# Kernel optimization log

Hardware: AMD Instinct MI355X
Metric: run time of the kernel (lower is better)

## Reference

```python
import jax, jax.numpy as jnp
import numpy as np

EMB_DIM = 128
WEIGHT_COL = 24

def setup_inputs() -> dict:
    key = jax.random.key(0)
    ks = jax.random.split(key, 9)
    B, S = 8, 4096
    s_in = 1.0 / np.sqrt(EMB_DIM)
    s_out = 1.0 / np.sqrt(WEIGHT_COL)
    return {
        "x": jax.random.normal(ks[0], (B, S, EMB_DIM), dtype=jnp.float32),
        "wQ": jax.random.uniform(ks[1], (EMB_DIM, WEIGHT_COL), jnp.float32, -s_in, s_in),
        "bQ": jax.random.uniform(ks[2], (WEIGHT_COL,), jnp.float32, -s_in, s_in),
        "wK": jax.random.uniform(ks[3], (EMB_DIM, WEIGHT_COL), jnp.float32, -s_in, s_in),
        "bK": jax.random.uniform(ks[4], (WEIGHT_COL,), jnp.float32, -s_in, s_in),
        "wV": jax.random.uniform(ks[5], (EMB_DIM, WEIGHT_COL), jnp.float32, -s_in, s_in),
        "bV": jax.random.uniform(ks[6], (WEIGHT_COL,), jnp.float32, -s_in, s_in),
        "wO": jax.random.uniform(ks[7], (WEIGHT_COL, EMB_DIM), jnp.float32, -s_out, s_out),
        "bO": jax.random.uniform(ks[8], (EMB_DIM,), jnp.float32, -s_out, s_out),
    }

def reference(x, wQ, bQ, wK, bK, wV, bV, wO, bO):
    # projections: [B,S,E] -> [B,S,D]
    Q = x @ wQ + bQ
    K = x @ wK + bK
    V = x @ wV + bV
    # NOTE: source scales by sqrt(emb_dim), not sqrt(weight_col)
    scale = 1.0 / np.sqrt(EMB_DIM).astype(np.float32)
    scores = jnp.einsum('bqd,bkd->bqk', Q, K) * scale  # [B,S,S]
    A = jax.nn.softmax(scores, axis=-1)
    H = jnp.einsum('bqk,bkd->bqd', A, V)               # [B,S,D]
    return H @ wO + bO                                  # [B,S,E]
```

## Files before the change

kernel.cpp:

```cpp
#include <hip/hip_runtime.h>
#include <hip/hip_fp16.h>


#define B_ 8
#define S_ 4096
#define E_ 128
#define D_ 24
#define N_ (B_ * S_)
#define SCALE 0.08838834764831845f
#define LOG2E 1.4426950408889634f

#define TK 128
#define KS_STRIDE 40
#define VS_STRIDE 136
#define HS_STRIDE 40
#define XS_STRIDE 136
#define OS_STRIDE 84

typedef __attribute__((ext_vector_type(8))) short bfrag;
typedef __attribute__((ext_vector_type(4))) float ffrag;

__device__ inline unsigned short f2bf(float f) {
    unsigned int x = __builtin_bit_cast(unsigned int, f);
    return (unsigned short)((x + 0x7fffu + ((x >> 16) & 1u)) >> 16);
}
__device__ inline unsigned int pack2h(float a, float b) {
    unsigned int ua = __builtin_bit_cast(unsigned int, a) + 0x8000u;
    unsigned int ub = __builtin_bit_cast(unsigned int, b) + 0x8000u;
    return __builtin_amdgcn_perm(ub, ua, 0x07060302);
}
__device__ inline unsigned int packh16(float a, float b) {
    return __builtin_bit_cast(unsigned int, __builtin_amdgcn_cvt_pkrtz(a, b));
}

__global__ __launch_bounds__(256) void prep_kernel(
    const float* __restrict__ wQ, const float* __restrict__ bQ,
    const float* __restrict__ wK, const float* __restrict__ bK,
    const float* __restrict__ wV, const float* __restrict__ bV,
    const float* __restrict__ wO,
    unsigned short* __restrict__ Wf, unsigned short* __restrict__ wOf,
    float* __restrict__ bqkv)
{
    const int gtid   = blockIdx.x * 256 + threadIdx.x;
    const int stride = gridDim.x * 256;
    const float qs = SCALE * LOG2E;
    for (int idx = gtid; idx < 4 * 5 * 512; idx += stride) {
        const int j    = idx & 7;
        const int lane = (idx >> 3) & 63;
        const int nt   = (idx >> 9) % 5;
        const int kt   = idx / 2560;
        const int n = nt * 16 + (lane & 15);
        const int k = kt * 32 + ((lane >> 4) << 3) + j;
        float v = 0.0f;
        if (n < 24)      v = wQ[k * 24 + n] * qs;
        else if (n < 48) v = wK[k * 24 + (n - 24)];
        else if (n < 72) v = wV[k * 24 + (n - 48)];
        Wf[idx] = f2bf(v);
    }
    for (int idx = gtid; idx < 8 * 512; idx += stride) {
        const int j    = idx & 7;
        const int lane = (idx >> 3) & 63;
        const int nt   = idx >> 9;
        const int k = ((lane >> 4) << 3) + j;
        const int e = nt * 16 + (lane & 15);
        wOf[idx] = (k < 24) ? f2bf(wO[k * 128 + e]) : (unsigned short)0;
    }
    if (gtid < 80) {
        float v = 0.0f;
        if (gtid < 24)      v = bQ[gtid] * qs;
        else if (gtid < 48) v = bK[gtid - 24];
        else if (gtid < 72) v = bV[gtid - 48];
        bqkv[gtid] = v;
    }
}

__global__ __launch_bounds__(256) void proj_kernel(
    const float* __restrict__ x, const unsigned short* __restrict__ Wf,
    const float* __restrict__ bqkv,
    unsigned short* __restrict__ Qbf, unsigned short* __restrict__ Kbf,
    unsigned short* __restrict__ Vt)
{
    __shared__ float smem[64 * OS_STRIDE];
    unsigned short* xs = (unsigned short*)smem;
    float* os = smem;

    const int tid  = threadIdx.x;
    const int lane = tid & 63;
    const int w    = tid >> 6;
    const int col  = lane & 15;
    const int quad = lane >> 4;
    const int rb   = blockIdx.x * 64;

    #pragma unroll
    for (int i = 0; i < 8; ++i) {
        const int idx = i * 256 + tid;
        const int row = idx >> 5, c4 = idx & 31;
        const float4 xv = *(const float4*)(x + (size_t)(rb + row) * 128 + c4 * 4);
        uint2 h;
        h.x = pack2h(xv.x, xv.y);
        h.y = pack2h(xv.z, xv.w);
        *(uint2*)(&xs[row * XS_STRIDE + c4 * 4]) = h;
    }

    bfrag Wfr[20];
    #pragma unroll
    for (int f = 0; f < 20; ++f)
        Wfr[f] = *(const bfrag*)(Wf + (f * 64 + lane) * 8);

    __syncthreads();

    ffrag acc[5];
    #pragma unroll
    for (int nt = 0; nt < 5; ++nt) acc[nt] = (ffrag){0.f, 0.f, 0.f, 0.f};

    #pragma unroll
    for (int kt = 0; kt < 4; ++kt) {
        const bfrag Af = *(const bfrag*)(&xs[(w * 16 + col) * XS_STRIDE + kt * 32 + quad * 8]);
        #pragma unroll
        for (int nt = 0; nt < 5; ++nt)
            acc[nt] = __builtin_amdgcn_mfma_f32_16x16x32_bf16(Af, Wfr[kt * 5 + nt], acc[nt], 0, 0, 0);
    }

    __syncthreads();

    #pragma unroll
    for (int nt = 0; nt < 5; ++nt) {
        const float bb = bqkv[nt * 16 + col];
        #pragma unroll
        for (int r = 0; r < 4; ++r)
            os[(w * 16 + quad * 4 + r) * OS_STRIDE + nt * 16 + col] = acc[nt][r] + bb;
    }
    __syncthreads();

    {
        const int half  = tid & 1;
        const int row   = (tid >> 1) & 63;
        const int isK   = tid >> 7;
        const int cbase = isK * 24;
        unsigned int pk[8];
        #pragma unroll
        for (int g = 0; g < 8; ++g) {
            const int c0 = half * 16 + g * 2;
            const float f0 = (c0     < 24) ? os[row * OS_STRIDE + cbase + c0]     : 0.0f;
            const float f1 = (c0 + 1 < 24) ? os[row * OS_STRIDE + cbase + c0 + 1] : 0.0f;
            pk[g] = pack2h(f0, f1);
        }
        unsigned short* dst = (isK ? Kbf : Qbf) + (size_t)(rb + row) * 32 + half * 16;
        *(uint4*)(dst)     = make_uint4(pk[0], pk[1], pk[2], pk[3]);
        *(uint4*)(dst + 8) = make_uint4(pk[4], pk[5], pk[6], pk[7]);
    }

    if (tid < 192) {
        const int d  = tid % 24;
        const int ch = tid / 24;
        unsigned int p[4];
        #pragma unroll
        for (int g = 0; g < 4; ++g) {
            const float f0 = os[(ch * 8 + g * 2 + 0) * OS_STRIDE + 48 + d];
            const float f1 = os[(ch * 8 + g * 2 + 1) * OS_STRIDE + 48 + d];
            p[g] = pack2h(f0, f1);
        }
        const int b = rb >> 12, s0 = rb & 4095;
        uint4* dst = (uint4*)(Vt + (((size_t)(b * 24 + d)) << 12) + s0 + ch * 8);
        *dst = make_uint4(p[0], p[1], p[2], p[3]);
    }
}

__global__ __launch_bounds__(512, 8) void attn_kernel(
    const unsigned short* __restrict__ Qbf, const unsigned short* __restrict__ Kbf,
    const unsigned short* __restrict__ Vt,
    __half* __restrict__ Opart, float* __restrict__ lpart)
{
    __shared__ unsigned short Ks[TK * KS_STRIDE];
    __shared__ unsigned short Vs[32 * VS_STRIDE];

    const int tid    = threadIdx.x;
    const int lane   = tid & 63;
    const int w      = tid >> 6;
    const int col    = lane & 15;
    const int quad   = lane >> 4;
    const int blk    = blockIdx.x;
    const int split  = blockIdx.y;
    const int nsp    = gridDim.y;
    const int kchunk = S_ / nsp;
    const int b      = blk >> 5;
    const int qbase  = blk * 128 + w * 16;

    if (tid < 16)
        *(uint4*)(&Vs[24 * VS_STRIDE + tid * 8]) =
            make_uint4(0x3F803F80u, 0x3F803F80u, 0x3F803F80u, 0x3F803F80u);

    const bfrag Qf = *(const bfrag*)(Qbf + (size_t)(qbase + col) * 32 + quad * 8);

    ffrag Ot0 = {0.f, 0.f, 0.f, 0.f};
    ffrag Ot1 = {0.f, 0.f, 0.f, 0.f};

    const unsigned short* Kbase = Kbf + ((size_t)(b * 4096) + split * kchunk) * 32;
    const unsigned short* Vbase = Vt + (size_t)(b * 24) * 4096 + split * kchunk;

    __syncthreads();

    for (int kb = 0; kb < kchunk; kb += TK) {
        {
            const int key = tid >> 2, ch = tid & 3;
            const uint4 t4 = *(const uint4*)(Kbase + (size_t)(kb + key) * 32 + ch * 8);
            const int row = (key & ~31) + (((key >> 2) & 1) << 4)
                          + (((key & 31) >> 3) << 2) + (key & 3);
            *(uint4*)(&Ks[row * KS_STRIDE + ch * 8]) = t4;
        }
        if (tid < 384) {
            const int d = tid >> 4, ch = tid & 15;
            const uint4 t4 = *(const uint4*)(Vbase + (size_t)d * 4096 + kb + ch * 8);
            *(uint4*)(&Vs[d * VS_STRIDE + ch * 8]) = t4;
        }
        __syncthreads();

        #pragma unroll
        for (int c2 = 0; c2 < 4; ++c2) {
            const bfrag Kfe = *(const bfrag*)(&Ks[(c2 * 32 + col) * KS_STRIDE + quad * 8]);
            const bfrag Kfo = *(const bfrag*)(&Ks[(c2 * 32 + 16 + col) * KS_STRIDE + quad * 8]);
            ffrag Se = {0.f, 0.f, 0.f, 0.f};
            ffrag So = {0.f, 0.f, 0.f, 0.f};
            Se = __builtin_amdgcn_mfma_f32_16x16x32_bf16(Kfe, Qf, Se, 0, 0, 0);
            So = __builtin_amdgcn_mfma_f32_16x16x32_bf16(Kfo, Qf, So, 0, 0, 0);
            union { bfrag f; unsigned int u[4]; } P;
            P.u[0] = pack2h(__builtin_amdgcn_exp2f(Se[0]), __builtin_amdgcn_exp2f(Se[1]));
            P.u[1] = pack2h(__builtin_amdgcn_exp2f(Se[2]), __builtin_amdgcn_exp2f(Se[3]));
            P.u[2] = pack2h(__builtin_amdgcn_exp2f(So[0]), __builtin_amdgcn_exp2f(So[1]));
            P.u[3] = pack2h(__builtin_amdgcn_exp2f(So[2]), __builtin_amdgcn_exp2f(So[3]));
            const bfrag Va0 = *(const bfrag*)(&Vs[col * VS_STRIDE + c2 * 32 + quad * 8]);
            const bfrag Va1 = *(const bfrag*)(&Vs[(16 + col) * VS_STRIDE + c2 * 32 + quad * 8]);
            Ot0 = __builtin_amdgcn_mfma_f32_16x16x32_bf16(Va0, P.f, Ot0, 0, 0, 0);
            Ot1 = __builtin_amdgcn_mfma_f32_16x16x32_bf16(Va1, P.f, Ot1, 0, 0, 0);
        }
        __syncthreads();
    }

    const size_t base = ((size_t)split * N_ + qbase + col) * 32;
    {
        uint2 s0;
        s0.x = packh16(Ot0[0], Ot0[1]);
        s0.y = packh16(Ot0[2], Ot0[3]);
        *(uint2*)(Opart + base + quad * 4) = s0;
    }
    if (quad < 2) {
        uint2 s1;
        s1.x = packh16(Ot1[0], Ot1[1]);
        s1.y = packh16(Ot1[2], Ot1[3]);
        *(uint2*)(Opart + base + 16 + quad * 4) = s1;
    }
    if (quad == 2)
        lpart[(size_t)split * N_ + qbase + col] = Ot1[0];
}

__global__ __launch_bounds__(256) void combine_kernel(
    const __half* __restrict__ Opart, const float* __restrict__ lpart,
    const unsigned short* __restrict__ wOf, const float* __restrict__ bO,
    float* __restrict__ out, int nsp)
{
    __shared__ unsigned short Hs[64 * HS_STRIDE];

    const int tid = threadIdx.x;
    const int qb  = blockIdx.x * 64;
    {
        const int ql = tid >> 2;
        const int c8 = (tid & 3) * 8;
        const int q  = qb + ql;
        float a[8] = {0.f, 0.f, 0.f, 0.f, 0.f, 0.f, 0.f, 0.f};
        if (c8 < 24) {
            for (int s = 0; s < nsp; ++s) {
                const __half2* p2 = (const __half2*)(Opart + ((size_t)s * N_ + q) * 32 + c8);
                #pragma unroll
                for (int j = 0; j < 4; ++j) {
                    const float2 f = __half22float2(p2[j]);
                    a[2 * j]     += f.x;
                    a[2 * j + 1] += f.y;
                }
            }
        }
        float ls = 0.f;
        for (int s = 0; s < nsp; ++s) ls += lpart[(size_t)s * N_ + q];
        const float inv = 1.0f / ls;
        uint4 pk;
        pk.x = pack2h(a[0] * inv, a[1] * inv);
        pk.y = pack2h(a[2] * inv, a[3] * inv);
        pk.z = pack2h(a[4] * inv, a[5] * inv);
        pk.w = pack2h(a[6] * inv, a[7] * inv);
        *(uint4*)(&Hs[ql * HS_STRIDE + c8]) = pk;
    }
    __syncthreads();

    const int lane = tid & 63;
    const int w    = tid >> 6;
    const int col  = lane & 15;
    const int quad = lane >> 4;
    const bfrag Hf = *(const bfrag*)(&Hs[(w * 16 + col) * HS_STRIDE + quad * 8]);
    #pragma unroll
    for (int nt = 0; nt < 8; ++nt) {
        const bfrag Wo = *(const bfrag*)(wOf + (nt * 64 + lane) * 8);
        ffrag C = {0.f, 0.f, 0.f, 0.f};
        C = __builtin_amdgcn_mfma_f32_16x16x32_bf16(Hf, Wo, C, 0, 0, 0);
        const float bo = bO[nt * 16 + col];
        #pragma unroll
        for (int r = 0; r < 4; ++r)
            out[(size_t)(qb + w * 16 + quad * 4 + r) * 128 + nt * 16 + col] = C[r] + bo;
    }
}

extern "C" void kernel_launch(void* const* d_in, const int* in_sizes, int n_in,
                              void* d_out, int out_size, void* d_ws, size_t ws_size,
                              hipStream_t stream) {
    const float* x  = (const float*)d_in[0];
    const float* wQ = (const float*)d_in[1];
    const float* bQ = (const float*)d_in[2];
    const float* wK = (const float*)d_in[3];
    const float* bK = (const float*)d_in[4];
    const float* wV = (const float*)d_in[5];
    const float* bV = (const float*)d_in[6];
    const float* wO = (const float*)d_in[7];
    const float* bO = (const float*)d_in[8];
    float* out = (float*)d_out;

    unsigned short* ws16 = (unsigned short*)d_ws;
    unsigned short* Qbf = ws16;
    unsigned short* Kbf = Qbf + (size_t)N_ * 32;
    unsigned short* Vt  = Kbf + (size_t)N_ * 32;
    unsigned short* Wf  = Vt + (size_t)B_ * 24 * S_;
    unsigned short* wOf = Wf + 4 * 5 * 512;
    float* bqkv = (float*)(wOf + 8 * 512);
    __half* Opart = (__half*)(bqkv + 80);
    const size_t baseBytes = (size_t)((char*)Opart - (char*)d_ws);

    int nsp = 4;
    while (nsp > 1) {
        const size_t need = baseBytes + (size_t)nsp * N_ * 32 * 2 + (size_t)nsp * N_ * 4;
        if (need <= ws_size) break;
        nsp >>= 1;
    }
    float* lpart = (float*)(Opart + (size_t)nsp * N_ * 32);

    prep_kernel<<<8, 256, 0, stream>>>(wQ, bQ, wK, bK, wV, bV, wO, Wf, wOf, bqkv);
    proj_kernel<<<N_ / 64, 256, 0, stream>>>(x, Wf, bqkv, Qbf, Kbf, Vt);
    attn_kernel<<<dim3(N_ / 128, nsp), 512, 0, stream>>>(Qbf, Kbf, Vt, Opart, lpart);
    combine_kernel<<<N_ / 64, 256, 0, stream>>>(Opart, lpart, wOf, bO, out, nsp);
}
```

Measured before the change: 123.0 us.

## Load K/V fragments directly from global memory, two query tiles per wave

The attention kernel no longer stages K and V tiles through LDS. Each wave now loads MFMA fragments straight from global memory, using a K row permutation that matches the previous shared-memory layout, so all __syncthreads are gone. Each wave handles 32 queries (two Q fragments) with 256-thread blocks, which reuses every loaded K/V fragment across two tiles. The V-transpose buffer is padded to 32 rows, and the projection kernel writes the ones-row used for the row-sum, so the attention kernel no longer initialises it. The trade-off is more global/L2 traffic and load latency with no explicit prefetch beyond a 2x unroll.

New measurement: 138.0 us. 1.12x slower.

```diff
diff --git a/kernel.cpp b/kernel.cpp
--- a/kernel.cpp
+++ b/kernel.cpp
@@ -10,9 +10,6 @@
 #define SCALE 0.08838834764831845f
 #define LOG2E 1.4426950408889634f
 
-#define TK 128
-#define KS_STRIDE 40
-#define VS_STRIDE 136
 #define HS_STRIDE 40
 #define XS_STRIDE 136
 #define OS_STRIDE 84
@@ -161,19 +158,21 @@
             p[g] = pack2h(f0, f1);
         }
         const int b = rb >> 12, s0 = rb & 4095;
-        uint4* dst = (uint4*)(Vt + (((size_t)(b * 24 + d)) << 12) + s0 + ch * 8);
+        uint4* dst = (uint4*)(Vt + (((size_t)(b * 32 + d)) << 12) + s0 + ch * 8);
         *dst = make_uint4(p[0], p[1], p[2], p[3]);
-    }
-}
-
-__global__ __launch_bounds__(512, 8) void attn_kernel(
+    } else if (tid < 200) {
+        const int ch = tid - 192;
+        const int b = rb >> 12, s0 = rb & 4095;
+        uint4* dst = (uint4*)(Vt + (((size_t)(b * 32 + 24)) << 12) + s0 + ch * 8);
+        *dst = make_uint4(0x3F803F80u, 0x3F803F80u, 0x3F803F80u, 0x3F803F80u);
+    }
+}
+
+__global__ __launch_bounds__(256, 4) void attn_kernel(
     const unsigned short* __restrict__ Qbf, const unsigned short* __restrict__ Kbf,
     const unsigned short* __restrict__ Vt,
     __half* __restrict__ Opart, float* __restrict__ lpart)
 {
-    __shared__ unsigned short Ks[TK * KS_STRIDE];
-    __shared__ unsigned short Vs[32 * VS_STRIDE];
-
     const int tid    = threadIdx.x;
     const int lane   = tid & 63;
     const int w      = tid >> 6;
@@ -181,76 +180,90 @@
     const int quad   = lane >> 4;
     const int blk    = blockIdx.x;
     const int split  = blockIdx.y;
-    const int nsp    = gridDim.y;
-    const int kchunk = S_ / nsp;
+    const int kchunk = S_ / gridDim.y;
     const int b      = blk >> 5;
-    const int qbase  = blk * 128 + w * 16;
-
-    if (tid < 16)
-        *(uint4*)(&Vs[24 * VS_STRIDE + tid * 8]) =
-            make_uint4(0x3F803F80u, 0x3F803F80u, 0x3F803F80u, 0x3F803F80u);
-
-    const bfrag Qf = *(const bfrag*)(Qbf + (size_t)(qbase + col) * 32 + quad * 8);
-
-    ffrag Ot0 = {0.f, 0.f, 0.f, 0.f};
-    ffrag Ot1 = {0.f, 0.f, 0.f, 0.f};
-
-    const unsigned short* Kbase = Kbf + ((size_t)(b * 4096) + split * kchunk) * 32;
-    const unsigned short* Vbase = Vt + (size_t)(b * 24) * 4096 + split * kchunk;
-
-    __syncthreads();
-
-    for (int kb = 0; kb < kchunk; kb += TK) {
+    const int qbase  = blk * 128 + w * 32;
+
+    const bfrag Qf0 = *(const bfrag*)(Qbf + (size_t)(qbase + col) * 32 + quad * 8);
+    const bfrag Qf1 = *(const bfrag*)(Qbf + (size_t)(qbase + 16 + col) * 32 + quad * 8);
+
+    const int keyE = ((col >> 2) << 3) + (col & 3);
+    const unsigned short* Kp =
+        Kbf + ((size_t)b * 4096 + (size_t)split * kchunk + keyE) * 32 + quad * 8;
+    const int d1 = (16 + col <= 24) ? (16 + col) : 24;
+    const unsigned short* Vp0 =
+        Vt + ((size_t)(b * 32 + col)) * 4096 + (size_t)split * kchunk + quad * 8;
+    const unsigned short* Vp1 =
+        Vt + ((size_t)(b * 32 + d1)) * 4096 + (size_t)split * kchunk + quad * 8;
+
+    ffrag O00 = {0.f,0.f,0.f,0.f};
+    ffrag O01 = {0.f,0.f,0.f,0.f};
+    ffrag O10 = {0.f,0.f,0.f,0.f};
+    ffrag O11 = {0.f,0.f,0.f,0.f};
+
+    #pragma unroll 2
+    for (int it = 0; it < kchunk; it += 32) {
+        const bfrag Kfe = *(const bfrag*)(Kp);
+        const bfrag Kfo = *(const bfrag*)(Kp + 128);
+        const bfrag Va0 = *(const bfrag*)(Vp0);
+        const bfrag Va1 = *(const bfrag*)(Vp1);
+        Kp += 1024; Vp0 += 32; Vp1 += 32;
+
         {
-            const int key = tid >> 2, ch = tid & 3;
-            const uint4 t4 = *(const uint4*)(Kbase + (size_t)(kb + key) * 32 + ch * 8);
-            const int row = (key & ~31) + (((key >> 2) & 1) << 4)
-                          + (((key & 31) >> 3) << 2) + (key & 3);
-            *(uint4*)(&Ks[row * KS_STRIDE + ch * 8]) = t4;
-        }
-        if (tid < 384) {
-            const int d = tid >> 4, ch = tid & 15;
-            const uint4 t4 = *(const uint4*)(Vbase + (size_t)d * 4096 + kb + ch * 8);
-            *(uint4*)(&Vs[d * VS_STRIDE + ch * 8]) = t4;
-        }
-        __syncthreads();
-
-        #pragma unroll
-        for (int c2 = 0; c2 < 4; ++c2) {
-            const bfrag Kfe = *(const bfrag*)(&Ks[(c2 * 32 + col) * KS_STRIDE + quad * 8]);
-            const bfrag Kfo = *(const bfrag*)(&Ks[(c2 * 32 + 16 + col) * KS_STRIDE + quad * 8]);
-            ffrag Se = {0.f, 0.f, 0.f, 0.f};
-            ffrag So = {0.f, 0.f, 0.f, 0.f};
-            Se = __builtin_amdgcn_mfma_f32_16x16x32_bf16(Kfe, Qf, Se, 0, 0, 0);
-            So = __builtin_amdgcn_mfma_f32_16x16x32_bf16(Kfo, Qf, So, 0, 0, 0);
+            ffrag Se = {0.f,0.f,0.f,0.f}, So = {0.f,0.f,0.f,0.f};
+            Se = __builtin_amdgcn_mfma_f32_16x16x32_bf16(Kfe, Qf0, Se, 0, 0, 0);
+            So = __builtin_amdgcn_mfma_f32_16x16x32_bf16(Kfo, Qf0, So, 0, 0, 0);
             union { bfrag f; unsigned int u[4]; } P;
             P.u[0] = pack2h(__builtin_amdgcn_exp2f(Se[0]), __builtin_amdgcn_exp2f(Se[1]));
             P.u[1] = pack2h(__builtin_amdgcn_exp2f(Se[2]), __builtin_amdgcn_exp2f(Se[3]));
             P.u[2] = pack2h(__builtin_amdgcn_exp2f(So[0]), __builtin_amdgcn_exp2f(So[1]));
             P.u[3] = pack2h(__builtin_amdgcn_exp2f(So[2]), __builtin_amdgcn_exp2f(So[3]));
-            const bfrag Va0 = *(const bfrag*)(&Vs[col * VS_STRIDE + c2 * 32 + quad * 8]);
-            const bfrag Va1 = *(const bfrag*)(&Vs[(16 + col) * VS_STRIDE + c2 * 32 + quad * 8]);
-            Ot0 = __builtin_amdgcn_mfma_f32_16x16x32_bf16(Va0, P.f, Ot0, 0, 0, 0);
-            Ot1 = __builtin_amdgcn_mfma_f32_16x16x32_bf16(Va1, P.f, Ot1, 0, 0, 0);
-        }
-        __syncthreads();
-    }
-
-    const size_t base = ((size_t)split * N_ + qbase + col) * 32;
+            O00 = __builtin_amdgcn_mfma_f32_16x16x32_bf16(Va0, P.f, O00, 0, 0, 0);
+            O01 = __builtin_amdgcn_mfma_f32_16x16x32_bf16(Va1, P.f, O01, 0, 0, 0);
+        }
+        {
+            ffrag Se = {0.f,0.f,0.f,0.f}, So = {0.f,0.f,0.f,0.f};
+            Se = __builtin_amdgcn_mfma_f32_16x16x32_bf16(Kfe, Qf1, Se, 0, 0, 0);
+            So = __builtin_amdgcn_mfma_f32_16x16x32_bf16(Kfo, Qf1, So, 0, 0, 0);
+            union { bfrag f; unsigned int u[4]; } P;
+            P.u[0] = pack2h(__builtin_amdgcn_exp2f(Se[0]), __builtin_amdgcn_exp2f(Se[1]));
+            P.u[1] = pack2h(__builtin_amdgcn_exp2f(Se[2]), __builtin_amdgcn_exp2f(Se[3]));
+            P.u[2] = pack2h(__builtin_amdgcn_exp2f(So[0]), __builtin_amdgcn_exp2f(So[1]));
+            P.u[3] = pack2h(__builtin_amdgcn_exp2f(So[2]), __builtin_amdgcn_exp2f(So[3]));
+            O10 = __builtin_amdgcn_mfma_f32_16x16x32_bf16(Va0, P.f, O10, 0, 0, 0);
+            O11 = __builtin_amdgcn_mfma_f32_16x16x32_bf16(Va1, P.f, O11, 0, 0, 0);
+        }
+    }
+
     {
+        const size_t base0 = ((size_t)split * N_ + qbase + col) * 32;
         uint2 s0;
-        s0.x = packh16(Ot0[0], Ot0[1]);
-        s0.y = packh16(Ot0[2], Ot0[3]);
-        *(uint2*)(Opart + base + quad * 4) = s0;
-    }
-    if (quad < 2) {
-        uint2 s1;
-        s1.x = packh16(Ot1[0], Ot1[1]);
-        s1.y = packh16(Ot1[2], Ot1[3]);
-        *(uint2*)(Opart + base + 16 + quad * 4) = s1;
-    }
-    if (quad == 2)
-        lpart[(size_t)split * N_ + qbase + col] = Ot1[0];
+        s0.x = packh16(O00[0], O00[1]);
+        s0.y = packh16(O00[2], O00[3]);
+        *(uint2*)(Opart + base0 + quad * 4) = s0;
+        if (quad < 2) {
+            uint2 s1;
+            s1.x = packh16(O01[0], O01[1]);
+            s1.y = packh16(O01[2], O01[3]);
+            *(uint2*)(Opart + base0 + 16 + quad * 4) = s1;
+        }
+        if (quad == 2)
+            lpart[(size_t)split * N_ + qbase + col] = O01[0];
+
+        const size_t base1 = base0 + 16 * 32;
+        uint2 t0;
+        t0.x = packh16(O10[0], O10[1]);
+        t0.y = packh16(O10[2], O10[3]);
+        *(uint2*)(Opart + base1 + quad * 4) = t0;
+        if (quad < 2) {
+            uint2 t1;
+            t1.x = packh16(O11[0], O11[1]);
+            t1.y = packh16(O11[2], O11[3]);
+            *(uint2*)(Opart + base1 + 16 + quad * 4) = t1;
+        }
+        if (quad == 2)
+            lpart[(size_t)split * N_ + qbase + 16 + col] = O11[0];
+    }
 }
 
 __global__ __launch_bounds__(256) void combine_kernel(
@@ -325,7 +338,7 @@
     unsigned short* Qbf = ws16;
     unsigned short* Kbf = Qbf + (size_t)N_ * 32;
     unsigned short* Vt  = Kbf + (size_t)N_ * 32;
-    unsigned short* Wf  = Vt + (size_t)B_ * 24 * S_;
+    unsigned short* Wf  = Vt + (size_t)B_ * 32 * S_;
     unsigned short* wOf = Wf + 4 * 5 * 512;
     float* bqkv = (float*)(wOf + 8 * 512);
     __half* Opart = (__half*)(bqkv + 80);
@@ -341,6 +354,6 @@
 
     prep_kernel<<<8, 256, 0, stream>>>(wQ, bQ, wK, bK, wV, bV, wO, Wf, wOf, bqkv);
     proj_kernel<<<N_ / 64, 256, 0, stream>>>(x, Wf, bqkv, Qbf, Kbf, Vt);
-    attn_kernel<<<dim3(N_ / 128, nsp), 512, 0, stream>>>(Qbf, Kbf, Vt, Opart, lpart);
+    attn_kernel<<<dim3(N_ / 128, nsp), 256, 0, stream>>>(Qbf, Kbf, Vt, Opart, lpart);
     combine_kernel<<<N_ / 64, 256, 0, stream>>>(Opart, lpart, wOf, bO, out, nsp);
 }
```
